# Optimization experiments

Measured on AMD Instinct MI355X. Metric: run time of the kernel, lower is better.

Reference implementation:

```python
import jax, jax.numpy as jnp
import numpy as np

B = 8192
D = 128
N_CLASSES = 100
TEMPERATURE = 0.1


def setup_inputs() -> dict:
    key = jax.random.key(0)
    k1, k2 = jax.random.split(key)
    feats = jax.random.normal(k1, (B, D), dtype=jnp.float32)
    # L2-normalise as the docstring assumes
    feats = feats / jnp.linalg.norm(feats, axis=1, keepdims=True)
    labels = jax.random.randint(k2, (B,), 0, N_CLASSES, dtype=jnp.int64)
    return {"features": feats, "labels": labels}


def reference(features, labels):
    features = features.astype(jnp.float32)
    b = features.shape[0]
    sim = (features @ features.T) / TEMPERATURE            # (B, B)
    labels_eq = labels[None, :] == labels[:, None]          # (B, B)
    self_mask = ~jnp.eye(b, dtype=bool)                     # (B, B), False on diag
    pos_mask = labels_eq & self_mask

    sim_max = jax.lax.stop_gradient(jnp.max(sim, axis=1, keepdims=True))
    logits = sim - sim_max                                  # (B, B)
    exp_logits = jnp.exp(logits) * self_mask.astype(jnp.float32)
    log_sum_exp = jnp.log(jnp.sum(exp_logits, axis=1, keepdims=True) + 1e-12)
    log_prob = logits - log_sum_exp                         # (B, B)

    n_positives = jnp.sum(pos_mask.astype(jnp.float32), axis=1)  # (B,)
    valid = n_positives > 0
    mean_log_prob = jnp.sum(pos_mask.astype(jnp.float32) * log_prob, axis=1) \
        / jnp.maximum(n_positives, 1.0)

    valid_f = valid.astype(jnp.float32)
    n_valid = jnp.sum(valid_f)
    loss = -jnp.sum(mean_log_prob * valid_f) / jnp.maximum(n_valid, 1.0)
    # match torch: return 0 if no anchor has a positive
    return jnp.where(n_valid > 0, loss, jnp.float32(0.0))
```

## Files before the change

### kernel.cpp

```cpp
#include <hip/hip_runtime.h>
#include <hip/hip_bf16.h>


#define BB 8192
#define DD 128
#define NC 8
#define COLCHUNK (BB / NC)
#define ITERS (COLCHUNK / 128)
#define TEMP_INV 10.0f
#define MSHIFT 10.5f
#define C1F 14.426950408889634f
#define C2F -15.148297929334116f

typedef __bf16 bf16x8 __attribute__((ext_vector_type(8)));
typedef float floatx4 __attribute__((ext_vector_type(4)));

__device__ inline float fast_exp2(float x) {
#if __has_builtin(__builtin_amdgcn_exp2f)
    return __builtin_amdgcn_exp2f(x);
#else
    return exp2f(x);
#endif
}

__device__ inline unsigned short f2bf(float f) {
    unsigned u = __float_as_uint(f);
    return (unsigned short)((u + 0x7FFFu + ((u >> 16) & 1u)) >> 16);
}

__device__ inline void gload_lds16(const void* g, void* l) {
    __builtin_amdgcn_global_load_lds(
        (const __attribute__((address_space(1))) void*)g,
        (__attribute__((address_space(3))) void*)l, 16, 0, 0);
}

__global__ __launch_bounds__(256) void supcon_convert(
    const void* __restrict__ fin, const void* __restrict__ lin,
    unsigned short* __restrict__ fbf, int* __restrict__ lab,
    float* __restrict__ accbuf)
{
    int lane = threadIdx.x & 63;
    unsigned ue = ((unsigned)((const unsigned short*)fin)[2 * lane]) << 16;
    float fe = __uint_as_float(ue);
    float ve = fe * fe;
    int odd_or = ((const int*)lin)[2 * lane + 1];
#pragma unroll
    for (int m = 1; m < 64; m <<= 1) {
        ve += __shfl_xor(ve, m, 64);
        odd_or |= __shfl_xor(odd_or, m, 64);
    }
    bool f_bf16 = (ve > 0.05f) && (ve < 4.0f);
    bool l_i64  = (odd_or == 0);

    int gid = blockIdx.x * 256 + threadIdx.x;
    if (!f_bf16) {
        float4 v = ((const float4*)fin)[gid];
        ushort4 o;
        o.x = f2bf(v.x); o.y = f2bf(v.y); o.z = f2bf(v.z); o.w = f2bf(v.w);
        ((ushort4*)fbf)[gid] = o;
    } else {
        ((ushort4*)fbf)[gid] = ((const ushort4*)fin)[gid];
    }
    if (blockIdx.x < 32) {
        int li = blockIdx.x * 256 + threadIdx.x;
        const int* L = (const int*)lin;
        lab[li] = l_i64 ? L[2 * li] : L[li];
    }
    if (blockIdx.x == 0 && threadIdx.x == 0) {
        accbuf[0] = 0.0f;
        accbuf[1] = 0.0f;
        ((unsigned*)accbuf)[2] = 0u;
    }
}

#define STAGE_B(itx, bsel)                                                   \
    {                                                                        \
        const unsigned char* gB =                                            \
            Fbc + (size_t)(colchunkbase + (itx) * 128) * 256;                \
        unsigned char* lb = &ldsB[bsel][0];                                  \
        _Pragma("unroll")                                                    \
        for (int r = 0; r < 8; ++r) {                                        \
            int off = r * 4096 + wid * 1024 + lane * 16;                     \
            int row = off >> 8;                                              \
            int g   = (off >> 4) & 15;                                       \
            int gs  = g ^ (row & 15);                                        \
            gload_lds16(gB + row * 256 + gs * 16,                            \
                        lb + r * 4096 + wid * 1024);                         \
        }                                                                    \
    }

__global__ __launch_bounds__(256, 2) void supcon_main(
    const unsigned short* __restrict__ Fb, const int* __restrict__ labels,
    float* __restrict__ e_part, float* __restrict__ p_part,
    float* __restrict__ diag)
{
    __shared__ unsigned char ldsB[2][32768];
    __shared__ float red[2][128][2];

    const int tid  = threadIdx.x;
    const int lane = tid & 63;
    const int wid  = tid >> 6;
    const int wrow = wid >> 1;
    const int wcol = wid & 1;
    const int quad = lane >> 4;
    const int l16  = lane & 15;

    const int chunk   = blockIdx.x;
    const int rowbase = blockIdx.y * 128;
    const int colchunkbase = chunk * COLCHUNK;

    const unsigned char* Fbc = (const unsigned char*)Fb;

    STAGE_B(0, 0);

    bf16x8 afrag[4][4];
#pragma unroll
    for (int ti = 0; ti < 4; ++ti) {
        int row = rowbase + wrow * 64 + ti * 16 + l16;
        const unsigned char* gA = Fbc + (size_t)row * 256 + quad * 16;
#pragma unroll
        for (int k = 0; k < 4; ++k)
            afrag[ti][k] = *(const bf16x8*)(gA + k * 64);
    }

    int lab_row[16];
#pragma unroll
    for (int ti = 0; ti < 4; ++ti)
#pragma unroll
        for (int r = 0; r < 4; ++r)
            lab_row[ti * 4 + r] = labels[rowbase + wrow * 64 + ti * 16 + quad * 4 + r];

    float e_acc[16], p_acc[16];
#pragma unroll
    for (int i = 0; i < 16; ++i) { e_acc[i] = 0.0f; p_acc[i] = 0.0f; }

    __syncthreads();

    int cur = 0;
    for (int it = 0; it < ITERS; ++it) {
        if (it + 1 < ITERS) STAGE_B(it + 1, cur ^ 1);

        int colbase = colchunkbase + it * 128;
        const unsigned char* lb = &ldsB[cur][0];

#pragma unroll
        for (int tj = 0; tj < 4; ++tj) {
            int coll = wcol * 64 + tj * 16 + l16;
            bf16x8 bfrag[4];
#pragma unroll
            for (int k = 0; k < 4; ++k) {
                int g  = k * 4 + quad;
                int gs = g ^ (coll & 15);
                bfrag[k] = *(const bf16x8*)(lb + coll * 256 + gs * 16);
            }
            floatx4 acc[4];
#pragma unroll
            for (int ti = 0; ti < 4; ++ti) acc[ti] = (floatx4){0.f, 0.f, 0.f, 0.f};
#pragma unroll
            for (int k = 0; k < 4; ++k)
#pragma unroll
                for (int ti = 0; ti < 4; ++ti)
                    acc[ti] = __builtin_amdgcn_mfma_f32_16x16x32_bf16(
                        afrag[ti][k], bfrag[k], acc[ti], 0, 0, 0);

            {
                int ctb = colbase + wcol * 64 + tj * 16;
                unsigned u = (unsigned)(ctb - (rowbase + wrow * 64));
                if (u < 64u) {
#pragma unroll
                    for (int ti2 = 0; ti2 < 4; ++ti2) {
                        if (u == (unsigned)(ti2 * 16)) {
#pragma unroll
                            for (int r = 0; r < 4; ++r)
                                if (l16 == quad * 4 + r)
                                    diag[ctb + l16] = acc[ti2][r];
                        }
                    }
                }
            }

            int lab_c = labels[colbase + coll];
#pragma unroll
            for (int ti = 0; ti < 4; ++ti) {
#pragma unroll
                for (int r = 0; r < 4; ++r) {
                    int i = ti * 4 + r;
                    float a  = acc[ti][r];
                    float ex = fast_exp2(__builtin_fmaf(a, C1F, C2F));
                    e_acc[i] += ex;
                    float peq = (lab_c == lab_row[i]) ? 1.0f : 0.0f;
                    p_acc[i] = __builtin_fmaf(peq, a, p_acc[i]);
                }
            }
        }
        __syncthreads();
        cur ^= 1;
    }

#pragma unroll
    for (int i = 0; i < 16; ++i) {
        float e = e_acc[i], p = p_acc[i];
#pragma unroll
        for (int m = 1; m < 16; m <<= 1) {
            e += __shfl_xor(e, m, 64);
            p += __shfl_xor(p, m, 64);
        }
        if (l16 == 0) {
            int row_local = wrow * 64 + (i >> 2) * 16 + quad * 4 + (i & 3);
            red[0][row_local][wcol] = e;
            red[1][row_local][wcol] = p;
        }
    }
    __syncthreads();

    if (tid < 128) {
        size_t idx = (size_t)chunk * BB + (rowbase + tid);
        e_part[idx] = red[0][tid][0] + red[0][tid][1];
        p_part[idx] = red[1][tid][0] + red[1][tid][1];
    }
}

__global__ __launch_bounds__(256) void supcon_reduce(
    const float* __restrict__ e_part, const float* __restrict__ p_part,
    const int* __restrict__ labels, const float* __restrict__ diag,
    float* __restrict__ accbuf, float* __restrict__ out)
{
    __shared__ int cnt[128];
    if (threadIdx.x < 128) cnt[threadIdx.x] = 0;
    __syncthreads();
    for (int i = threadIdx.x; i < BB; i += 256)
        atomicAdd(&cnt[labels[i]], 1);
    __syncthreads();

    int row = blockIdx.x * 256 + threadIdx.x;
    float e = 0.f, p = 0.f;
#pragma unroll
    for (int c = 0; c < NC; ++c) {
        size_t idx = (size_t)c * BB + row;
        e += e_part[idx]; p += p_part[idx];
    }
    float d = diag[row];
    e -= fast_exp2(__builtin_fmaf(d, C1F, C2F));
    p -= d;
    int n_i = cnt[labels[row]] - 1;

    float contrib = 0.f, vld = 0.f;
    if (n_i > 0) {
        vld = 1.0f;
        contrib = -(p * TEMP_INV / (float)n_i - MSHIFT - logf(e));
    }
#pragma unroll
    for (int m = 1; m < 64; m <<= 1) {
        contrib += __shfl_xor(contrib, m, 64);
        vld     += __shfl_xor(vld, m, 64);
    }
    __shared__ float rl[4], rv[4];
    int lane = threadIdx.x & 63, w = threadIdx.x >> 6;
    if (lane == 0) { rl[w] = contrib; rv[w] = vld; }
    __syncthreads();
    if (threadIdx.x == 0) {
        float L = rl[0] + rl[1] + rl[2] + rl[3];
        float V = rv[0] + rv[1] + rv[2] + rv[3];
        atomicAdd(&accbuf[0], L);
        atomicAdd(&accbuf[1], V);
        __threadfence();
        unsigned t = atomicAdd((unsigned*)accbuf + 2, 1u);
        if (t == 31u) {
            float Ls = atomicAdd(&accbuf[0], 0.0f);
            float Vs = atomicAdd(&accbuf[1], 0.0f);
            out[0] = (Vs > 0.5f) ? (Ls / Vs) : 0.0f;
        }
    }
}

extern "C" void kernel_launch(void* const* d_in, const int* in_sizes, int n_in,
                              void* d_out, int out_size, void* d_ws, size_t ws_size,
                              hipStream_t stream)
{
    const void* Fin = d_in[0];
    const void* Lin = d_in[1];

    unsigned short* fbf = (unsigned short*)d_ws;
    int*   lab      = (int*)((char*)d_ws + (size_t)BB * DD * 2);
    float* e_part   = (float*)((char*)lab + (size_t)BB * 4);
    float* p_part   = e_part + (size_t)NC * BB;
    float* diag     = p_part + (size_t)NC * BB;
    float* accbuf   = diag + BB;

    supcon_convert<<<BB * DD / 4 / 256, 256, 0, stream>>>(Fin, Lin, fbf, lab, accbuf);

    dim3 grid(NC, BB / 128);
    supcon_main<<<grid, 256, 0, stream>>>(fbf, lab, e_part, p_part, diag);

    supcon_reduce<<<32, 256, 0, stream>>>(e_part, p_part, lab, diag, accbuf, (float*)d_out);
}
```

Baseline: 97.24 us.

## Compute positive-pair sums via per-class feature sums instead of inside GEMM loop

Uses linearity: the sum of sim over same-class columns equals the row feature dotted with its class-sum vector. A new kernel builds the per-class feature sums with LDS atomics, and the reduce kernel does a 128-wide dot product per row. This removes label loads, compares and FMAs from the main B×B epilogue. The main kernel also moves to 16 column chunks with 64-column tiles and smaller LDS buffers. The cost is an extra launch and an atomic class-sum pass, plus bf16 rounding effects in the class sums.

```diff
diff --git a/kernel.cpp b/kernel.cpp
--- a/kernel.cpp
+++ b/kernel.cpp
@@ -4,9 +4,11 @@
 
 #define BB 8192
 #define DD 128
-#define NC 8
+#define NCLS 100
+#define NC 16
 #define COLCHUNK (BB / NC)
-#define ITERS (COLCHUNK / 128)
+#define TILEC 64
+#define ITERS (COLCHUNK / TILEC)
 #define TEMP_INV 10.0f
 #define MSHIFT 10.5f
 #define C1F 14.426950408889634f
@@ -28,6 +30,10 @@
     return (unsigned short)((u + 0x7FFFu + ((u >> 16) & 1u)) >> 16);
 }
 
+__device__ inline float bf2f(unsigned short s) {
+    return __uint_as_float(((unsigned)s) << 16);
+}
+
 __device__ inline void gload_lds16(const void* g, void* l) {
     __builtin_amdgcn_global_load_lds(
         (const __attribute__((address_space(1))) void*)g,
@@ -37,7 +43,7 @@
 __global__ __launch_bounds__(256) void supcon_convert(
     const void* __restrict__ fin, const void* __restrict__ lin,
     unsigned short* __restrict__ fbf, int* __restrict__ lab,
-    float* __restrict__ accbuf)
+    float* __restrict__ g, float* __restrict__ accbuf)
 {
     int lane = threadIdx.x & 63;
     unsigned ue = ((unsigned)((const unsigned short*)fin)[2 * lane]) << 16;
@@ -66,36 +72,61 @@
         const int* L = (const int*)lin;
         lab[li] = l_i64 ? L[2 * li] : L[li];
     }
-    if (blockIdx.x == 0 && threadIdx.x == 0) {
-        accbuf[0] = 0.0f;
-        accbuf[1] = 0.0f;
-        ((unsigned*)accbuf)[2] = 0u;
-    }
+    if (blockIdx.x == 0) {
+        for (int i = threadIdx.x; i < NCLS * DD; i += 256) g[i] = 0.0f;
+        if (threadIdx.x == 0) {
+            accbuf[0] = 0.0f;
+            accbuf[1] = 0.0f;
+            ((unsigned*)accbuf)[2] = 0u;
+        }
+    }
+}
+
+#define CS_BLOCKS 16
+#define CS_ROWS (BB / CS_BLOCKS)
+__global__ __launch_bounds__(256) void supcon_classsum(
+    const unsigned short* __restrict__ Fb, const int* __restrict__ lab,
+    float* __restrict__ g)
+{
+    __shared__ float gl[NCLS * DD];
+    for (int i = threadIdx.x; i < NCLS * DD; i += 256) gl[i] = 0.0f;
+    __syncthreads();
+
+    int base = blockIdx.x * CS_ROWS;
+    int d  = threadIdx.x & 127;
+    int rh = threadIdx.x >> 7;
+    for (int j0 = 0; j0 < CS_ROWS; j0 += 2) {
+        int j = base + j0 + rh;
+        int c = lab[j];
+        float v = bf2f(Fb[(size_t)j * DD + d]);
+        atomicAdd(&gl[c * DD + d], v);
+    }
+    __syncthreads();
+    for (int i = threadIdx.x; i < NCLS * DD; i += 256)
+        atomicAdd(&g[i], gl[i]);
 }
 
 #define STAGE_B(itx, bsel)                                                   \
     {                                                                        \
         const unsigned char* gB =                                            \
-            Fbc + (size_t)(colchunkbase + (itx) * 128) * 256;                \
+            Fbc + (size_t)(colchunkbase + (itx) * TILEC) * 256;              \
         unsigned char* lb = &ldsB[bsel][0];                                  \
         _Pragma("unroll")                                                    \
-        for (int r = 0; r < 8; ++r) {                                        \
-            int off = r * 4096 + wid * 1024 + lane * 16;                     \
+        for (int r = 0; r < 4; ++r) {                                        \
+            int off = r * 4096 + tid * 16;                                   \
             int row = off >> 8;                                              \
-            int g   = (off >> 4) & 15;                                       \
-            int gs  = g ^ (row & 15);                                        \
-            gload_lds16(gB + row * 256 + gs * 16,                            \
-                        lb + r * 4096 + wid * 1024);                         \
+            int gg  = (off >> 4) & 15;                                       \
+            int gs  = gg ^ (row & 15);                                       \
+            gload_lds16(gB + row * 256 + gs * 16, lb + off);                 \
         }                                                                    \
     }
 
 __global__ __launch_bounds__(256, 2) void supcon_main(
-    const unsigned short* __restrict__ Fb, const int* __restrict__ labels,
-    float* __restrict__ e_part, float* __restrict__ p_part,
-    float* __restrict__ diag)
-{
-    __shared__ unsigned char ldsB[2][32768];
-    __shared__ float red[2][128][2];
+    const unsigned short* __restrict__ Fb,
+    float* __restrict__ e_part, float* __restrict__ diag)
+{
+    __shared__ unsigned char ldsB[2][16384];
+    __shared__ float red[128][2];
 
     const int tid  = threadIdx.x;
     const int lane = tid & 63;
@@ -123,16 +154,9 @@
             afrag[ti][k] = *(const bf16x8*)(gA + k * 64);
     }
 
-    int lab_row[16];
-#pragma unroll
-    for (int ti = 0; ti < 4; ++ti)
-#pragma unroll
-        for (int r = 0; r < 4; ++r)
-            lab_row[ti * 4 + r] = labels[rowbase + wrow * 64 + ti * 16 + quad * 4 + r];
-
-    float e_acc[16], p_acc[16];
-#pragma unroll
-    for (int i = 0; i < 16; ++i) { e_acc[i] = 0.0f; p_acc[i] = 0.0f; }
+    float e_acc[16];
+#pragma unroll
+    for (int i = 0; i < 16; ++i) e_acc[i] = 0.0f;
 
     __syncthreads();
 
@@ -140,17 +164,17 @@
     for (int it = 0; it < ITERS; ++it) {
         if (it + 1 < ITERS) STAGE_B(it + 1, cur ^ 1);
 
-        int colbase = colchunkbase + it * 128;
+        int colbase = colchunkbase + it * TILEC;
         const unsigned char* lb = &ldsB[cur][0];
 
 #pragma unroll
-        for (int tj = 0; tj < 4; ++tj) {
-            int coll = wcol * 64 + tj * 16 + l16;
+        for (int tj = 0; tj < 2; ++tj) {
+            int coll = wcol * 32 + tj * 16 + l16;
             bf16x8 bfrag[4];
 #pragma unroll
             for (int k = 0; k < 4; ++k) {
-                int g  = k * 4 + quad;
-                int gs = g ^ (coll & 15);
+                int gg = k * 4 + quad;
+                int gs = gg ^ (coll & 15);
                 bfrag[k] = *(const bf16x8*)(lb + coll * 256 + gs * 16);
             }
             floatx4 acc[4];
@@ -164,7 +188,7 @@
                         afrag[ti][k], bfrag[k], acc[ti], 0, 0, 0);
 
             {
-                int ctb = colbase + wcol * 64 + tj * 16;
+                int ctb = colbase + wcol * 32 + tj * 16;
                 unsigned u = (unsigned)(ctb - (rowbase + wrow * 64));
                 if (u < 64u) {
 #pragma unroll
@@ -179,17 +203,12 @@
                 }
             }
 
-            int lab_c = labels[colbase + coll];
 #pragma unroll
             for (int ti = 0; ti < 4; ++ti) {
 #pragma unroll
                 for (int r = 0; r < 4; ++r) {
-                    int i = ti * 4 + r;
-                    float a  = acc[ti][r];
-                    float ex = fast_exp2(__builtin_fmaf(a, C1F, C2F));
-                    e_acc[i] += ex;
-                    float peq = (lab_c == lab_row[i]) ? 1.0f : 0.0f;
-                    p_acc[i] = __builtin_fmaf(peq, a, p_acc[i]);
+                    float a = acc[ti][r];
+                    e_acc[ti * 4 + r] += fast_exp2(__builtin_fmaf(a, C1F, C2F));
                 }
             }
         }
@@ -199,30 +218,26 @@
 
 #pragma unroll
     for (int i = 0; i < 16; ++i) {
-        float e = e_acc[i], p = p_acc[i];
-#pragma unroll
-        for (int m = 1; m < 16; m <<= 1) {
-            e += __shfl_xor(e, m, 64);
-            p += __shfl_xor(p, m, 64);
-        }
+        float e = e_acc[i];
+#pragma unroll
+        for (int m = 1; m < 16; m <<= 1) e += __shfl_xor(e, m, 64);
         if (l16 == 0) {
             int row_local = wrow * 64 + (i >> 2) * 16 + quad * 4 + (i & 3);
-            red[0][row_local][wcol] = e;
-            red[1][row_local][wcol] = p;
+            red[row_local][wcol] = e;
         }
     }
     __syncthreads();
 
     if (tid < 128) {
         size_t idx = (size_t)chunk * BB + (rowbase + tid);
-        e_part[idx] = red[0][tid][0] + red[0][tid][1];
-        p_part[idx] = red[1][tid][0] + red[1][tid][1];
+        e_part[idx] = red[tid][0] + red[tid][1];
     }
 }
 
 __global__ __launch_bounds__(256) void supcon_reduce(
-    const float* __restrict__ e_part, const float* __restrict__ p_part,
-    const int* __restrict__ labels, const float* __restrict__ diag,
+    const float* __restrict__ e_part, const unsigned short* __restrict__ Fb,
+    const int* __restrict__ labels, const float* __restrict__ g,
+    const float* __restrict__ diag,
     float* __restrict__ accbuf, float* __restrict__ out)
 {
     __shared__ int cnt[128];
@@ -233,16 +248,36 @@
     __syncthreads();
 
     int row = blockIdx.x * 256 + threadIdx.x;
-    float e = 0.f, p = 0.f;
-#pragma unroll
-    for (int c = 0; c < NC; ++c) {
-        size_t idx = (size_t)c * BB + row;
-        e += e_part[idx]; p += p_part[idx];
-    }
+    float e = 0.f;
+#pragma unroll
+    for (int c = 0; c < NC; ++c)
+        e += e_part[(size_t)c * BB + row];
+
+    int cls = labels[row];
+
+    const unsigned short* fr = Fb + (size_t)row * DD;
+    const float* gr = g + cls * DD;
+    float p0 = 0.f, p1 = 0.f;
+#pragma unroll
+    for (int q = 0; q < 8; ++q) {
+        uint4  u  = ((const uint4*)fr)[q];
+        float4 ga = ((const float4*)gr)[2 * q];
+        float4 gb = ((const float4*)gr)[2 * q + 1];
+        p0 = __builtin_fmaf(__uint_as_float(u.x << 16),          ga.x, p0);
+        p1 = __builtin_fmaf(__uint_as_float(u.x & 0xFFFF0000u),  ga.y, p1);
+        p0 = __builtin_fmaf(__uint_as_float(u.y << 16),          ga.z, p0);
+        p1 = __builtin_fmaf(__uint_as_float(u.y & 0xFFFF0000u),  ga.w, p1);
+        p0 = __builtin_fmaf(__uint_as_float(u.z << 16),          gb.x, p0);
+        p1 = __builtin_fmaf(__uint_as_float(u.z & 0xFFFF0000u),  gb.y, p1);
+        p0 = __builtin_fmaf(__uint_as_float(u.w << 16),          gb.z, p0);
+        p1 = __builtin_fmaf(__uint_as_float(u.w & 0xFFFF0000u),  gb.w, p1);
+    }
+    float p = p0 + p1;
+
     float d = diag[row];
     e -= fast_exp2(__builtin_fmaf(d, C1F, C2F));
     p -= d;
-    int n_i = cnt[labels[row]] - 1;
+    int n_i = cnt[cls] - 1;
 
     float contrib = 0.f, vld = 0.f;
     if (n_i > 0) {
@@ -283,14 +318,16 @@
     unsigned short* fbf = (unsigned short*)d_ws;
     int*   lab      = (int*)((char*)d_ws + (size_t)BB * DD * 2);
     float* e_part   = (float*)((char*)lab + (size_t)BB * 4);
-    float* p_part   = e_part + (size_t)NC * BB;
-    float* diag     = p_part + (size_t)NC * BB;
-    float* accbuf   = diag + BB;
-
-    supcon_convert<<<BB * DD / 4 / 256, 256, 0, stream>>>(Fin, Lin, fbf, lab, accbuf);
+    float* diag     = e_part + (size_t)NC * BB;
+    float* g        = diag + BB;
+    float* accbuf   = g + NCLS * DD;
+
+    supcon_convert<<<BB * DD / 4 / 256, 256, 0, stream>>>(Fin, Lin, fbf, lab, g, accbuf);
+
+    supcon_classsum<<<CS_BLOCKS, 256, 0, stream>>>(fbf, lab, g);
 
     dim3 grid(NC, BB / 128);
-    supcon_main<<<grid, 256, 0, stream>>>(fbf, lab, e_part, p_part, diag);
-
-    supcon_reduce<<<32, 256, 0, stream>>>(e_part, p_part, lab, diag, accbuf, (float*)d_out);
-}
+    supcon_main<<<grid, 256, 0, stream>>>(fbf, e_part, diag);
+
+    supcon_reduce<<<32, 256, 0, stream>>>(e_part, fbf, lab, g, diag, accbuf, (float*)d_out);
+}
```

Result: slower. 188.9 us (+94.2%).
